# Kernel tuning notes

Hardware: AMD Instinct MI355X
Metric: run time of the kernel (lower is better)

## Reference

```python
import jax, jax.numpy as jnp
import numpy as np
import math

N = 1500; E = 24000; C_IN = 16; H = 64; NUM_LAYERS = 10; RATIO = 0.9
NEG = -1e9


def setup_inputs() -> dict:
    key = jax.random.key(0)
    ks = jax.random.split(key, 40)
    it = iter(range(40))
    def nrm(shape, scale=0.1):
        return jax.random.normal(ks[next(it)], shape, dtype=jnp.float32) * scale
    src = jax.random.randint(ks[next(it)], (E,), 0, N, dtype=jnp.int32)
    off = jax.random.randint(ks[next(it)], (E,), 1, N, dtype=jnp.int32)
    dst = (src + off) % N  # no self loops in the raw edge list
    return dict(
        x=nrm((N, C_IN), 1.0),
        edge_src=src, edge_dst=dst,
        W1=nrm((C_IN, H // 2)), b1=jnp.zeros((H // 2,), jnp.float32),
        W2=nrm((H // 2, H)), b2=jnp.zeros((H,), jnp.float32),
        W3=nrm((H, H)), b3=jnp.zeros((H,), jnp.float32),
        Wrel=nrm((NUM_LAYERS - 1, H, H)), brel=jnp.zeros((NUM_LAYERS - 1, H), jnp.float32),
        Wroot=nrm((NUM_LAYERS - 1, H, H)),
        pW=nrm((4, H, H)), pb=jnp.zeros((4, H), jnp.float32),
        leW1=nrm((4, H, 1)), leb1=jnp.zeros((4, 1), jnp.float32),
        leW2=nrm((4, H, 1)),
        leW3=nrm((4, H, 1)), leb3=jnp.zeros((4, 1), jnp.float32),
        linW1=nrm((NUM_LAYERS * H, H)), linb1=jnp.zeros((H,), jnp.float32),
        linW2=nrm((H, 10)), linb2=jnp.zeros((10,), jnp.float32),
    )


def _seg_mean(vals, idx, n):
    s = jax.ops.segment_sum(vals, idx, num_segments=n)
    c = jax.ops.segment_sum(jnp.ones((idx.shape[0],), vals.dtype), idx, num_segments=n)
    return s / jnp.maximum(c, 1.0)[:, None]


def _feast(x, W, b, srcL, dstL, n):
    # FeaStConv with heads=1: softmax over a single head == 1 -> mean of lin(x_j) + bias
    return _seg_mean((x @ W)[srcL], dstL, n) + b


def _gconv_sparse(x, src, dst, Wr, br, Wo, n):
    return _seg_mean(x[src], dst, n) @ Wr + br + x @ Wo


def _gconv_dense(x, A, Wr, br, Wo):
    # mean aggregation: divide weighted sum by count of (nonzero) in-edges
    Mf = (A != 0).astype(x.dtype)
    agg = (A.T @ x) / jnp.maximum(Mf.sum(0), 1.0)[:, None]
    return agg @ Wr + br + x @ Wo


def _topk_pool(xc, fitness, ratio):
    k = int(math.ceil(ratio * xc.shape[0]))
    fit_k, perm = jax.lax.top_k(fitness, k)
    return xc[perm] * fit_k[:, None], perm


def _asap_sparse(x, src, dst, pW, pb, leW1, leb1, leW2, leW3, leb3):
    n = x.shape[0]
    ar = jnp.arange(n, dtype=src.dtype)
    srcL = jnp.concatenate([src, ar])  # add remaining self loops (weight 1)
    dstL = jnp.concatenate([dst, ar])
    xq = jax.ops.segment_max(x[srcL], dstL, num_segments=n) @ pW + pb
    s = jax.nn.leaky_relu(jnp.sum(xq[dstL] * x[srcL], -1), 0.2)
    m = jax.ops.segment_max(s, dstL, num_segments=n)
    e = jnp.exp(s - m[dstL])
    score = e / jax.ops.segment_sum(e, dstL, num_segments=n)[dstL]
    xc = jax.ops.segment_sum(x[srcL] * score[:, None], dstL, num_segments=n)
    # LEConv fitness score (edge weight = 1)
    a = xc @ leW1 + leb1
    b = xc @ leW2
    agg = jax.ops.segment_sum(a[srcL] - b[dstL], dstL, num_segments=n)
    fitness = jax.nn.sigmoid((agg + xc @ leW3 + leb3)[:, 0])
    x_new, perm = _topk_pool(xc, fitness, RATIO)
    S = jnp.zeros((n, n), x.dtype).at[srcL, dstL].add(score)
    A = jnp.zeros((n, n), x.dtype).at[srcL, dstL].add(1.0)
    Sp = S[:, perm]
    A_new = Sp.T @ A @ Sp
    k = A_new.shape[0]
    return x_new, A_new * (1.0 - jnp.eye(k, dtype=x.dtype))  # remove diag


def _asap_dense(x, A, pW, pb, leW1, leb1, leW2, leW3, leb3):
    n = x.shape[0]
    A = A + jnp.diag((jnp.diag(A) == 0).astype(A.dtype))  # add remaining self loops
    M = A != 0
    Mf = M.astype(x.dtype)
    xq = jnp.max(jnp.where(M[:, :, None], x[:, None, :], NEG), axis=0) @ pW + pb  # [n,H]
    Sc = jnp.where(M, jax.nn.leaky_relu(x @ xq.T, 0.2), NEG)  # [j,i]
    m = Sc.max(0)
    e = jnp.where(M, jnp.exp(Sc - m), 0.0)
    score = e / e.sum(0)
    xc = score.T @ x
    a = xc @ leW1 + leb1
    b = xc @ leW2
    agg = Mf.T @ a - Mf.sum(0)[:, None] * b
    fitness = jax.nn.sigmoid((agg + xc @ leW3 + leb3)[:, 0])
    x_new, perm = _topk_pool(xc, fitness, RATIO)
    Sp = score[:, perm]
    A_new = Sp.T @ A @ Sp
    k = A_new.shape[0]
    return x_new, A_new * (1.0 - jnp.eye(k, dtype=x.dtype))


def _forward(x, edge_src, edge_dst, W1, b1, W2, b2, W3, b3, Wrel, brel, Wroot,
             pW, pb, leW1, leb1, leW2, leW3, leb3, linW1, linb1, linW2, linb2):
    n = x.shape[0]
    ar = jnp.arange(n, dtype=edge_src.dtype)
    srcL = jnp.concatenate([edge_src, ar])  # FeaStConv add_self_loops=True
    dstL = jnp.concatenate([edge_dst, ar])
    x = jax.nn.elu(_feast(x, W1, b1, srcL, dstL, n))
    x = jax.nn.elu(_feast(x, W2, b2, srcL, dstL, n))
    x = jax.nn.elu(_feast(x, W3, b3, srcL, dstL, n))
    xs = [x.mean(0, keepdims=True)]  # single graph -> global_mean_pool == mean
    A = None
    for i in range(NUM_LAYERS - 1):
        if A is None:
            x = jax.nn.relu(_gconv_sparse(x, edge_src, edge_dst, Wrel[i], brel[i], Wroot[i], x.shape[0]))
        else:
            x = jax.nn.relu(_gconv_dense(x, A, Wrel[i], brel[i], Wroot[i]))
        xs.append(x.mean(0, keepdims=True))
        if i % 2 == 0 and i < NUM_LAYERS - 2:
            p = i // 2
            args = (pW[p], pb[p], leW1[p], leb1[p], leW2[p], leW3[p], leb3[p])
            if A is None:
                x, A = _asap_sparse(x, edge_src, edge_dst, *args)
            else:
                x, A = _asap_dense(x, A, *args)
    h = jnp.concatenate(xs, axis=-1)  # [1, NUM_LAYERS*H] jumping-knowledge cat
    h = jax.nn.relu(h @ linW1 + linb1)
    return jax.nn.log_softmax(h @ linW2 + linb2, axis=-1)


def reference(x, edge_src, edge_dst, W1, b1, W2, b2, W3, b3, Wrel, brel, Wroot,
              pW, pb, leW1, leb1, leW2, leW3, leb3, linW1, linb1, linW2, linb2):
    return _forward(x, edge_src, edge_dst, W1, b1, W2, b2, W3, b3, Wrel, brel, Wroot,
                    pW, pb, leW1, leb1, leW2, leW3, leb3, linW1, linb1, linW2, linb2)
```

## Files before the change

### kernel.cpp

```cpp
#include <hip/hip_runtime.h>
#include <math.h>

#define NEGV -1000000000.0f

typedef short short8 __attribute__((ext_vector_type(8)));
typedef float floatx4 __attribute__((ext_vector_type(4)));

__device__ __forceinline__ float sigm(float x){ return 1.0f/(1.0f+expf(-x)); }
__device__ __forceinline__ void edge_sd(int e,const int* src,const int* dst,int E,int& s,int& d){
  if(e<E){ s=src[e]; d=dst[e]; } else { s=e-E; d=s; }
}
__device__ __forceinline__ ushort bf16rn(float x){
  unsigned u = __float_as_uint(x);
  unsigned r = (u + 0x7fffu + ((u>>16)&1u)) >> 16;
  return (ushort)r;
}
__device__ __forceinline__ float bf16f(ushort h){ return __uint_as_float(((unsigned)h)<<16); }

__global__ void k_zero(float* __restrict__ p, size_t n){
  size_t i = (size_t)blockIdx.x*256 + threadIdx.x;
  if (i < n) p[i] = 0.0f;
}

__global__ void k_split3(const float* __restrict__ src,int R,int Cs,int ld,
                         ushort* __restrict__ dst,int Cp,int bmode){
  int idx = blockIdx.x*256+threadIdx.x;
  if (idx >= R*Cp) return;
  int r = idx / Cp, c = idx - r*Cp;
  float x = (c < Cs) ? src[(size_t)r*ld + c] : 0.0f;
  ushort h = bf16rn(x);
  ushort l = bf16rn(x - bf16f(h));
  size_t base = (size_t)r*(3*Cp) + c;
  dst[base]        = h;
  dst[base + Cp]   = bmode ? l : h;
  dst[base + 2*Cp] = bmode ? h : l;
}
__global__ void k_split3_Tdual(const float* __restrict__ src,int Rs,int Cs,int ld,
                               const int* __restrict__ gperm,const float* __restrict__ cscale,
                               const float* __restrict__ emax,
                               ushort* __restrict__ dstA,ushort* __restrict__ dstB,
                               ushort* __restrict__ dstCpad,int Kp){
  __shared__ float t[32][33];
  int tx = threadIdx.x & 31, ty = threadIdx.x >> 5;
  int kb = blockIdx.y*32, xb = blockIdx.x*32;
  int x = xb + tx;
  int gx = (x < Cs) ? gperm[x] : 0;
#pragma unroll
  for (int i=0;i<4;i++){
    int k = kb + ty + i*8;
    t[ty+i*8][tx] = (k < Rs && x < Cs) ? src[(size_t)k*ld + gx] : 0.0f;
  }
  __syncthreads();
  const int K3 = 3*Kp;
#pragma unroll
  for (int i=0;i<4;i++){
    int xo = xb + ty + i*8, ko = kb + tx;
    if (xo < Cs){
      float v = 0.0f;
      if (ko < Rs){
        int g = gperm[xo];
        v = expf(t[tx][ty+i*8] - emax[g]) * cscale[g];
      }
      ushort h = bf16rn(v);
      ushort l = bf16rn(v - bf16f(h));
      size_t base = (size_t)xo*K3 + ko;
      dstA[base] = h; dstA[base+Kp] = h; dstA[base+2*Kp] = l;
      dstB[base] = h; dstB[base+Kp] = l; dstB[base+2*Kp] = h;
      if (ko >= Rs){ dstCpad[base]=0; dstCpad[base+Kp]=0; dstCpad[base+2*Kp]=0; }
    }
  }
}

template<int EPI>
__global__ __launch_bounds__(256) void k_gemm_mfma(
    const ushort* __restrict__ A, const ushort* __restrict__ B,
    float* __restrict__ C, int ldc, int M, int N, int K3,
    const float* __restrict__ mask, int ldm)
{
  __shared__ ushort As[2][64][72];
  __shared__ ushort Bs[2][64][72];
  const int tid = threadIdx.x;
  const int m0 = blockIdx.y*64, n0 = blockIdx.x*64;
  const int w = tid>>6, lane = tid&63;
  const int lo4 = lane&15, quad = lane>>4;
  const int sr = tid>>2, sseg = tid&3;

  floatx4 acc[4];
#pragma unroll
  for(int c=0;c<4;c++){ acc[c][0]=0.f; acc[c][1]=0.f; acc[c][2]=0.f; acc[c][3]=0.f; }

  const size_t arow = (size_t)(m0+sr)*K3;
  const size_t brow = (size_t)(n0+sr)*K3;
  const bool aval = (m0+sr) < M;
  const bool bval = (n0+sr) < N;

  uint4 av0 = make_uint4(0,0,0,0), av1 = make_uint4(0,0,0,0);
  uint4 bv0 = make_uint4(0,0,0,0), bv1 = make_uint4(0,0,0,0);
  if (aval){ av0 = *(const uint4*)(A + arow + sseg*8);
             av1 = *(const uint4*)(A + arow + 32 + sseg*8); }
  if (bval){ bv0 = *(const uint4*)(B + brow + sseg*8);
             bv1 = *(const uint4*)(B + brow + 32 + sseg*8); }
  *(uint4*)&As[0][sr][sseg*8] = av0; *(uint4*)&As[0][sr][32+sseg*8] = av1;
  *(uint4*)&Bs[0][sr][sseg*8] = bv0; *(uint4*)&Bs[0][sr][32+sseg*8] = bv1;
  __syncthreads();

  const int T = K3 >> 6;
  for (int i=0;i<T;i++){
    const int cb = i & 1;
    if (i+1 < T){
      const int k0 = (i+1)<<6;
      av0 = make_uint4(0,0,0,0); av1 = make_uint4(0,0,0,0);
      bv0 = make_uint4(0,0,0,0); bv1 = make_uint4(0,0,0,0);
      if (aval){ av0 = *(const uint4*)(A + arow + k0 + sseg*8);
                 av1 = *(const uint4*)(A + arow + k0 + 32 + sseg*8); }
      if (bval){ bv0 = *(const uint4*)(B + brow + k0 + sseg*8);
                 bv1 = *(const uint4*)(B + brow + k0 + 32 + sseg*8); }
    }
    short8 af0 = *(const short8*)&As[cb][16*w + lo4][quad*8];
    short8 af1 = *(const short8*)&As[cb][16*w + lo4][32+quad*8];
#pragma unroll
    for (int c=0;c<4;c++){
      short8 bf0 = *(const short8*)&Bs[cb][16*c + lo4][quad*8];
      acc[c] = __builtin_amdgcn_mfma_f32_16x16x32_bf16(af0, bf0, acc[c], 0, 0, 0);
      short8 bf1 = *(const short8*)&Bs[cb][16*c + lo4][32+quad*8];
      acc[c] = __builtin_amdgcn_mfma_f32_16x16x32_bf16(af1, bf1, acc[c], 0, 0, 0);
    }
    if (i+1 < T){
      __syncthreads();
      *(uint4*)&As[1-cb][sr][sseg*8] = av0; *(uint4*)&As[1-cb][sr][32+sseg*8] = av1;
      *(uint4*)&Bs[1-cb][sr][sseg*8] = bv0; *(uint4*)&Bs[1-cb][sr][32+sseg*8] = bv1;
      __syncthreads();
    }
  }

#pragma unroll
  for (int c=0;c<4;c++){
    const int gn = n0 + 16*c + lo4;
#pragma unroll
    for (int r=0;r<4;r++){
      const int gm = m0 + 16*w + quad*4 + r;
      if (gm < M && gn < N){
        float v = acc[c][r];
        if (EPI==1) v = (mask[(size_t)gm*ldm+gn] != 0.0f || gm==gn) ? (v > 0.0f ? v : 0.2f*v) : NEGV;
        if (EPI==2 && gm==gn) v = 0.0f;
        C[(size_t)gm*ldc+gn] = v;
      }
    }
  }
}

__global__ __launch_bounds__(256) void k_gemm_mfma_tb(
    const ushort* __restrict__ A, const ushort* __restrict__ B,
    ushort* __restrict__ Cb, int Kp, int M, int N, int K3)
{
  __shared__ ushort As[2][64][72];
  __shared__ ushort Bs[2][64][72];
  const int tid = threadIdx.x;
  const int m0 = blockIdx.y*64, n0 = blockIdx.x*64;
  const int w = tid>>6, lane = tid&63;
  const int lo4 = lane&15, quad = lane>>4;
  const int sr = tid>>2, sseg = tid&3;

  floatx4 acc[4];
#pragma unroll
  for(int c=0;c<4;c++){ acc[c][0]=0.f; acc[c][1]=0.f; acc[c][2]=0.f; acc[c][3]=0.f; }

  const size_t arow = (size_t)(m0+sr)*K3;
  const size_t brow = (size_t)(n0+sr)*K3;
  const bool aval = (m0+sr) < M;
  const bool bval = (n0+sr) < N;

  uint4 av0 = make_uint4(0,0,0,0), av1 = make_uint4(0,0,0,0);
  uint4 bv0 = make_uint4(0,0,0,0), bv1 = make_uint4(0,0,0,0);
  if (aval){ av0 = *(const uint4*)(A + arow + sseg*8);
             av1 = *(const uint4*)(A + arow + 32 + sseg*8); }
  if (bval){ bv0 = *(const uint4*)(B + brow + sseg*8);
             bv1 = *(const uint4*)(B + brow + 32 + sseg*8); }
  *(uint4*)&As[0][sr][sseg*8] = av0; *(uint4*)&As[0][sr][32+sseg*8] = av1;
  *(uint4*)&Bs[0][sr][sseg*8] = bv0; *(uint4*)&Bs[0][sr][32+sseg*8] = bv1;
  __syncthreads();

  const int T = K3 >> 6;
  for (int i=0;i<T;i++){
    const int cb = i & 1;
    if (i+1 < T){
      const int k0 = (i+1)<<6;
      av0 = make_uint4(0,0,0,0); av1 = make_uint4(0,0,0,0);
      bv0 = make_uint4(0,0,0,0); bv1 = make_uint4(0,0,0,0);
      if (aval){ av0 = *(const uint4*)(A + arow + k0 + sseg*8);
                 av1 = *(const uint4*)(A + arow + k0 + 32 + sseg*8); }
      if (bval){ bv0 = *(const uint4*)(B + brow + k0 + sseg*8);
                 bv1 = *(const uint4*)(B + brow + k0 + 32 + sseg*8); }
    }
    short8 af0 = *(const short8*)&As[cb][16*w + lo4][quad*8];
    short8 af1 = *(const short8*)&As[cb][16*w + lo4][32+quad*8];
#pragma unroll
    for (int c=0;c<4;c++){
      short8 bf0 = *(const short8*)&Bs[cb][16*c + lo4][quad*8];
      acc[c] = __builtin_amdgcn_mfma_f32_16x16x32_bf16(af0, bf0, acc[c], 0, 0, 0);
      short8 bf1 = *(const short8*)&Bs[cb][16*c + lo4][32+quad*8];
      acc[c] = __builtin_amdgcn_mfma_f32_16x16x32_bf16(af1, bf1, acc[c], 0, 0, 0);
    }
    if (i+1 < T){
      __syncthreads();
      *(uint4*)&As[1-cb][sr][sseg*8] = av0; *(uint4*)&As[1-cb][sr][32+sseg*8] = av1;
      *(uint4*)&Bs[1-cb][sr][sseg*8] = bv0; *(uint4*)&Bs[1-cb][sr][32+sseg*8] = bv1;
      __syncthreads();
    }
  }

  const int K3o = 3*Kp;
#pragma unroll
  for (int c=0;c<4;c++){
    const int gn = n0 + 16*c + lo4;
    if (gn < N){
#pragma unroll
      for (int r=0;r<4;r++){
        const int gm = m0 + 16*w + quad*4 + r;
        if (gm < M){
          size_t base = (size_t)gn*K3o + gm;
          float sp = bf16f(B[base]) + bf16f(B[base+Kp]);
          float v = acc[c][r] + sp;
          ushort h = bf16rn(v);
          ushort l = bf16rn(v - bf16f(h));
          Cb[base] = h; Cb[base+Kp] = l; Cb[base+2*Kp] = h;
        }
      }
    }
  }
}

template<bool MAXM, bool COUNT, bool EXPM, bool SELF>
__global__ __launch_bounds__(256) void k_skinny(
    const float* __restrict__ A, int lda,
    const float* __restrict__ X,
    const float* __restrict__ mcol,
    float* __restrict__ P, int* __restrict__ cntp,
    int M, int K, int kchunk)
{
  __shared__ float As[16][68];
  __shared__ float Xs[16][68];
  const int tid = threadIdx.x;
  const int m0 = blockIdx.y * 64;
  const int tmb = (tid & 15) * 4, tnb = (tid >> 4) * 4;
  float acc[4][4];
  int cacc[4] = {0,0,0,0};
#pragma unroll
  for (int i=0;i<4;i++)
#pragma unroll
    for (int j=0;j<4;j++) acc[i][j] = MAXM ? NEGV : 0.0f;

  const int kstart = blockIdx.z * kchunk;
  int kend = kstart + kchunk; if (kend > K) kend = K;
  const int ml = tid & 63, tb = tid >> 6;
  const bool mvalid = (m0 + ml) < M;
  float mc = 0.0f;
  if (EXPM && mvalid) mc = mcol[m0 + ml];

  for (int k0 = kstart; k0 < kend; k0 += 16) {
#pragma unroll
    for (int s=0;s<4;s++) {
      const int tk = tb + s*4;
      float va = 0.0f, vx = 0.0f;
      if ((k0+tk) < K) {
        if (mvalid){
          va = A[(size_t)(k0+tk)*lda + m0 + ml];
          if (EXPM) va = expf(va - mc);
        }
        vx = X[(size_t)(k0+tk)*64 + ml];
      }
      As[tk][ml] = va;
      Xs[tk][ml] = vx;
    }
    __syncthreads();
#pragma unroll
    for (int kk=0; kk<16; kk++) {
      const float4 a4 = *(const float4*)&As[kk][tmb];
      const float4 b4 = *(const float4*)&Xs[kk][tnb];
      const float av[4] = {a4.x,a4.y,a4.z,a4.w};
      const float bv[4] = {b4.x,b4.y,b4.z,b4.w};
#pragma unroll
      for (int i=0;i<4;i++){
        if (COUNT) cacc[i] += (av[i] != 0.0f) ? 1 : 0;
#pragma unroll
        for (int j=0;j<4;j++) {
          if (MAXM) acc[i][j] = fmaxf(acc[i][j], av[i] != 0.0f ? bv[j] : NEGV);
          else      acc[i][j] = fmaf(av[i], bv[j], acc[i][j]);
        }
      }
    }
    __syncthreads();
  }

  const size_t slab = (size_t)blockIdx.z * M * 64;
#pragma unroll
  for (int i=0;i<4;i++){
    const int m = m0 + tmb + i;
    if (m < M){
#pragma unroll
      for (int j=0;j<4;j++){
        float v = acc[i][j];
        if (SELF) v = fmaxf(v, X[(size_t)m*64 + tnb + j]);
        P[slab + (size_t)m*64 + tnb + j] = v;
      }
    }
  }
  if (COUNT && tnb == 0){
#pragma unroll
    for (int i=0;i<4;i++){
      const int m = m0 + tmb + i;
      if (m < M) cntp[blockIdx.z*M + m] = cacc[i];
    }
  }
}

__global__ __launch_bounds__(256) void k_poolq(
    const float* __restrict__ SEGP,const int* __restrict__ cntp8,int Z,
    const float* __restrict__ pWp,const float* __restrict__ pbp,
    const float* __restrict__ X,
    ushort* __restrict__ dstA,ushort* __restrict__ dstB,
    float* __restrict__ cntP,int n)
{
  __shared__ float xq[4][65];
  const int tid = threadIdx.x;
  const int r = tid>>6, j = tid&63;
  const int i = blockIdx.x*4 + r;
  float v = NEGV;
  if (i < n){
    for(int z=0;z<Z;z++) v = fmaxf(v, SEGP[(size_t)z*n*64 + (size_t)i*64 + j]);
    if (j == 0){
      int c=1; for(int z=0;z<Z;z++) c += cntp8[z*n+i];
      cntP[i] = (float)c;
    }
  }
  xq[r][j] = v;
  __syncthreads();
  if (i < n){
    float s = pbp[j];
    for(int q=0;q<64;q++) s = fmaf(xq[r][q], pWp[q*64+j], s);
    size_t base = (size_t)i*192 + j;
    ushort h = bf16rn(s), l = bf16rn(s - bf16f(h));
    dstB[base] = h; dstB[base+64] = l; dstB[base+128] = h;
    float x = X[(size_t)i*64 + j];
    h = bf16rn(x); l = bf16rn(x - bf16f(h));
    dstA[base] = h; dstA[base+64] = h; dstA[base+128] = l;
  }
}

__global__ __launch_bounds__(256) void k_gconv_fuse(
    const float* __restrict__ SEGP,const int* __restrict__ cntp8,int Z,
    const float* __restrict__ Wrel,const float* __restrict__ brel,
    const float* __restrict__ X,const float* __restrict__ Wroot,
    float* __restrict__ XN,int n,float* __restrict__ meanacc,float inv_n)
{
  __shared__ float agg_s[4][65];
  __shared__ float xrow[4][65];
  __shared__ float cnt_s[4];
  const int tid = threadIdx.x;
  const int r = tid>>6, j = tid&63;
  const int i = blockIdx.x*4 + r;
  float a = 0.0f;
  if (i < n){
    for(int z=0;z<Z;z++) a += SEGP[(size_t)z*n*64 + (size_t)i*64 + j];
    xrow[r][j] = X[(size_t)i*64 + j];
    if (j == 0){
      int c=0; for(int z=0;z<Z;z++) c += cntp8[z*n+i];
      cnt_s[r] = (float)(c>1?c:1);
    }
  }
  agg_s[r][j] = a;
  __syncthreads();
  float v = 0.0f;
  if (i < n){
    float acc=0.0f, rt=0.0f;
    for(int q=0;q<64;q++){
      acc = fmaf(agg_s[r][q], Wrel[q*64+j], acc);
      rt  = fmaf(xrow[r][q],  Wroot[q*64+j], rt);
    }
    v = fmaxf(acc/cnt_s[r] + brel[j] + rt, 0.0f);
    XN[(size_t)i*64 + j] = v;
  }
  __syncthreads();
  agg_s[r][j] = v;
  __syncthreads();
  if (r == 0) atomicAdd(&meanacc[j], (agg_s[0][j]+agg_s[1][j]+agg_s[2][j]+agg_s[3][j])*inv_n);
}

__global__ __launch_bounds__(256) void k_smax_fused(const float* __restrict__ S,int n,
                                                    float* __restrict__ mcol,float* __restrict__ invd){
  __shared__ float red[16][17];
  const int jc = threadIdx.x & 15, rg = threadIdx.x >> 4;
  const int j = blockIdx.x*16 + jc;
  float m = -3.0e38f;
  if (j < n)
    for(int i=rg;i<n;i+=16) m = fmaxf(m, S[(size_t)i*n+j]);
  red[rg][jc] = m;
  __syncthreads();
  for(int s=8;s>0;s>>=1){
    if(rg<s) red[rg][jc] = fmaxf(red[rg][jc], red[rg+s][jc]);
    __syncthreads();
  }
  const float mc = red[0][jc];
  __syncthreads();
  float sum = 0.0f;
  if (j < n)
    for(int i=rg;i<n;i+=16) sum += expf(S[(size_t)i*n+j]-mc);
  red[rg][jc] = sum;
  __syncthreads();
  for(int s=8;s>0;s>>=1){
    if(rg<s) red[rg][jc] += red[rg+s][jc];
    __syncthreads();
  }
  if(rg==0 && j<n){ mcol[j]=mc; invd[j]=1.0f/red[0][jc]; }
}

__global__ __launch_bounds__(256) void k_xcabc_dense(
    const float* __restrict__ SEGP,int Z,const float* __restrict__ invd,
    float* __restrict__ XC,
    const float* __restrict__ w1,const float* bb1,const float* __restrict__ w2,
    const float* __restrict__ w3,const float* bb3,
    float* aN,float* bN,float* cN,int* pcnt,int n)
{
  __shared__ float xc[4][65];
  const int tid = threadIdx.x;
  const int r = tid>>6, j = tid&63;
  const int i = blockIdx.x*4 + r;
  if (blockIdx.x==0 && tid==0) *pcnt = 0;
  float v = 0.0f;
  if (i < n){
    for(int z=0;z<Z;z++) v += SEGP[(size_t)z*n*64 + (size_t)i*64 + j];
    v *= invd[i];
    XC[(size_t)i*64+j] = v;
  }
  xc[r][j] = v;
  __syncthreads();
  if (i < n && j < 3){
    float s = (j==0)?bb1[0]:((j==2)?bb3[0]:0.0f);
    const float* w = (j==0)?w1:((j==1)?w2:w3);
    for(int q=0;q<64;q++) s = fmaf(xc[r][q], w[q], s);
    if(j==0) aN[i]=s; else if(j==1) bN[i]=s; else cN[i]=s;
  }
}

__global__ void k_aggcol(const float* __restrict__ A,const float* __restrict__ aN,
                         float* __restrict__ aggp,int n){
  int idx = blockIdx.x*256+threadIdx.x; if(idx>=n*16) return;
  int j = idx % n, c = idx / n;
  int i0 = (int)(((long long)n*c)/16), i1 = (int)(((long long)n*(c+1))/16);
  float s = 0.0f;
  for(int i=i0;i<i1;i++) if(A[(size_t)i*n + j] != 0.0f) s += aN[i];
  aggp[c*n + j] = s;
}

template<int MODE>
__global__ __launch_bounds__(256) void k_rank_fused(
    const float* __restrict__ fit_in,
    const float* __restrict__ aggp,const float* __restrict__ cntP,
    const float* __restrict__ aN,const float* __restrict__ bN,const float* __restrict__ cN,
    const float* __restrict__ XC,float* __restrict__ XN,
    int n,int k,int* pcnt,int* perm)
{
  __shared__ float fs[1504];
  const int tid = threadIdx.x;
  for(int u=tid; u<n; u+=256){
    float f;
    if (MODE==0) f = fit_in[u];
    else {
      float a = aN[u];
      for(int c=0;c<16;c++) a += aggp[c*n+u];
      f = sigm(a - cntP[u]*bN[u] + cN[u]);
    }
    fs[u] = f;
  }
  __syncthreads();
  const int v = blockIdx.x*256+tid; if(v>=n) return;
  const float fv = fs[v]; int r = 0;
  for(int u=0;u<n;u++){ float fu = fs[u]; r += (fu > fv || (fu == fv && u < v)) ? 1 : 0; }
  if (r < k){
    int p = atomicAdd(pcnt,1);
    perm[p] = v;
    const float* src = XC + (size_t)v*64;
    float* d = XN + (size_t)p*64;
    for(int h=0;h<64;h++) d[h] = src[h]*fv;
  }
}

__global__ void k_deg(const int* __restrict__ src,const int* __restrict__ dst,int* indeg,int* outdeg,int E){
  int e = blockIdx.x*256+threadIdx.x; if(e>=E) return;
  atomicAdd(&indeg[dst[e]],1); atomicAdd(&outdeg[src[e]],1);
}
__global__ __launch_bounds__(256) void k_prefix2(const int* __restrict__ indeg,const int* __restrict__ outdeg,
                          int* offD,int* curD,int* offS,int* curS,int n){
  __shared__ int ds[1504];
  const int* dsrc = blockIdx.y ? outdeg : indeg;
  for(int u=threadIdx.x; u<n; u+=256) ds[u] = dsrc[u];
  __syncthreads();
  int t = blockIdx.x*256+threadIdx.x; if(t>n) return;
  int s = 0;
  for(int u=0;u<t;u++) s += ds[u]+1;
  if (blockIdx.y){ offS[t]=s; if(t<n) curS[t]=s; }
  else           { offD[t]=s; if(t<n) curD[t]=s; }
}
__global__ void k_csr_fill2(const int* src,const int* dst,
                            int* curS,int* colS,int* eidS,
                            int* curD,int* rowD,int* eidD,int E,int n){
  int e = blockIdx.x*256+threadIdx.x; if(e>=E+n) return;
  int s,d; edge_sd(e,src,dst,E,s,d);
  int p = atomicAdd(&curS[s],1); colS[p]=d; eidS[p]=e;
  int q = atomicAdd(&curD[d],1); rowD[q]=s; eidD[q]=e;
}

__global__ void k_mm_small(const float* __restrict__ A,const float* __restrict__ W,
                           const float* __restrict__ b,float* __restrict__ C,
                           int M,int K,int Np,int act){
  int idx = blockIdx.x*256+threadIdx.x; if(idx>=M*Np) return;
  int m = idx/Np, j = idx - m*Np;
  float s = b ? b[j] : 0.0f;
  const float* a = A + (size_t)m*K;
  for(int q=0;q<K;q++) s = fmaf(a[q], W[(size_t)q*Np + j], s);
  if(act==1) s = fmaxf(s, 0.0f);
  C[idx] = s;
}

__global__ void k_feast_gf(const float* __restrict__ Y,const int* __restrict__ offD,
                           const int* __restrict__ rowD,
                           const float* __restrict__ b,float* X,int n,int H,
                           float* __restrict__ meanacc,float inv_n){
  __shared__ float ms[4][64];
  int idx = blockIdx.x*256+threadIdx.x;
  float v = 0.0f;
  if(idx<n*H){
    int i = idx/H, h = idx - i*H;
    int p0 = offD[i], p1 = offD[i+1];
    float s = 0.0f;
    for(int p=p0;p<p1;p++) s += Y[(size_t)rowD[p]*H + h];
    float t = s/(float)(p1-p0) + b[h];
    v = t > 0.0f ? t : (expf(t)-1.0f);
    X[idx] = v;
  }
  if(meanacc){
    int r = threadIdx.x>>6, j = threadIdx.x&63;
    ms[r][j] = (idx<n*H) ? v : 0.0f;
    __syncthreads();
    if(r==0) atomicAdd(&meanacc[j], (ms[0][j]+ms[1][j]+ms[2][j]+ms[3][j])*inv_n);
  }
}

__global__ __launch_bounds__(256) void k_gconv_sparse_f(
    const float* __restrict__ X,const int* __restrict__ offD,const int* __restrict__ rowD,
    const int* __restrict__ eidD,int E,
    const float* __restrict__ Wrel,const float* __restrict__ brel,
    const float* __restrict__ Wroot,
    float* __restrict__ XN,int n,float* __restrict__ meanacc,float inv_n)
{
  __shared__ float agg_s[4][65];
  __shared__ float xrow[4][65];
  __shared__ float cnt_s[4];
  const int tid = threadIdx.x;
  const int r = tid>>6, j = tid&63;
  const int i = blockIdx.x*4 + r;
  float a = 0.0f;
  if (i < n){
    int p0 = offD[i], p1 = offD[i+1], c = 0;
    for(int p=p0;p<p1;p++){
      if (eidD[p] < E){ a += X[(size_t)rowD[p]*64 + j]; c++; }
    }
    xrow[r][j] = X[(size_t)i*64 + j];
    if (j == 0) cnt_s[r] = (float)(c>1?c:1);
  }
  agg_s[r][j] = a;
  __syncthreads();
  float v = 0.0f;
  if (i < n){
    float acc=0.0f, rt=0.0f;
    for(int q=0;q<64;q++){
      acc = fmaf(agg_s[r][q], Wrel[q*64+j], acc);
      rt  = fmaf(xrow[r][q],  Wroot[q*64+j], rt);
    }
    v = fmaxf(acc/cnt_s[r] + brel[j] + rt, 0.0f);
    XN[(size_t)i*64 + j] = v;
  }
  __syncthreads();
  agg_s[r][j] = v;
  __syncthreads();
  if (r == 0) atomicAdd(&meanacc[j], (agg_s[0][j]+agg_s[1][j]+agg_s[2][j]+agg_s[3][j])*inv_n);
}

__global__ __launch_bounds__(256) void k_xqmaxq(
    const float* __restrict__ X,const int* __restrict__ offD,const int* __restrict__ rowD,
    const float* __restrict__ pWp,const float* __restrict__ pbp,
    float* __restrict__ XQ2,int n)
{
  __shared__ float xq[4][65];
  const int tid = threadIdx.x;
  const int r = tid>>6, j = tid&63;
  const int i = blockIdx.x*4 + r;
  float v = -3.0e38f;
  if (i < n){
    int p0 = offD[i], p1 = offD[i+1];
    for(int p=p0;p<p1;p++) v = fmaxf(v, X[(size_t)rowD[p]*64 + j]);
  }
  xq[r][j] = v;
  __syncthreads();
  if (i < n){
    float s = pbp[j];
    for(int q=0;q<64;q++) s = fmaf(xq[r][q], pWp[q*64+j], s);
    XQ2[(size_t)i*64+j] = s;
  }
}

__global__ void k_edge_score(const int* __restrict__ src,const int* __restrict__ dst,
                             const float* __restrict__ XQ2,const float* __restrict__ X,
                             float* sE,int E,int n){
  int e = blockIdx.x*256+threadIdx.x; if(e>=E+n) return;
  int s,d; edge_sd(e,src,dst,E,s,d);
  const float* q = XQ2 + (size_t)d*64;
  const float* x = X + (size_t)s*64;
  float acc = 0.0f;
  for(int h=0;h<64;h++) acc = fmaf(q[h], x[h], acc);
  sE[e] = acc > 0.0f ? acc : 0.2f*acc;
}

__global__ void k_dstsoft(const int* __restrict__ offD,const int* __restrict__ eidD,
                          const float* __restrict__ sE,float* __restrict__ scE,int n){
  int i = blockIdx.x*256+threadIdx.x; if(i>=n) return;
  int p0 = offD[i], p1 = offD[i+1];
  float m = -3.0e38f;
  for(int p=p0;p<p1;p++) m = fmaxf(m, sE[eidD[p]]);
  float d = 0.0f;
  for(int p=p0;p<p1;p++) d += expf(sE[eidD[p]]-m);
  float inv = 1.0f/d;
  for(int p=p0;p<p1;p++){ int e = eidD[p]; scE[e] = expf(sE[e]-m)*inv; }
}

__global__ __launch_bounds__(256) void k_xcabc0(
    const int* __restrict__ offD,const int* __restrict__ rowD,const int* __restrict__ eidD,
    const float* __restrict__ scE,const float* __restrict__ X,
    float* __restrict__ XC,
    const float* __restrict__ w1,const float* bb1,const float* __restrict__ w2,
    const float* __restrict__ w3,const float* bb3,
    float* aN,float* bN,float* cN,int* pcnt,int n)
{
  __shared__ float xc[4][65];
  const int tid = threadIdx.x;
  const int r = tid>>6, j = tid&63;
  const int i = blockIdx.x*4 + r;
  if (blockIdx.x==0 && tid==0) *pcnt = 0;
  float v = 0.0f;
  if (i < n){
    int p0 = offD[i], p1 = offD[i+1];
    for(int p=p0;p<p1;p++) v += scE[eidD[p]] * X[(size_t)rowD[p]*64 + j];
    XC[(size_t)i*64+j] = v;
  }
  xc[r][j] = v;
  __syncthreads();
  if (i < n && j < 3){
    float s = (j==0)?bb1[0]:((j==2)?bb3[0]:0.0f);
    const float* w = (j==0)?w1:((j==1)?w2:w3);
    for(int q=0;q<64;q++) s = fmaf(xc[r][q], w[q], s);
    if(j==0) aN[i]=s; else if(j==1) bN[i]=s; else cN[i]=s;
  }
}

__global__ void k_aggfit0(const int* __restrict__ offD,const int* __restrict__ rowD,
                          const float* aN,const float* bN,const float* cN,
                          float* fit,int n){
  int i = blockIdx.x*256+threadIdx.x; if(i>=n) return;
  int p0 = offD[i], p1 = offD[i+1];
  float s = 0.0f;
  for(int p=p0;p<p1;p++) s += aN[rowD[p]];
  fit[i] = sigm(s - (float)(p1-p0)*bN[i] + cN[i]);
}

__global__ void k_stage1n(const int* src,const int* dst,const int* __restrict__ offS,
                          const int* __restrict__ colS,const int* __restrict__ eidS,
                          const float* __restrict__ scE,
                          float* R,int E,int n){
  int e = blockIdx.x*256+threadIdx.x; if(e>=E+n) return;
  int i,j; edge_sd(e,src,dst,E,i,j);
  int p0 = offS[j], p1 = offS[j+1];
  float* Ri = R + (size_t)i*n;
  for(int p=p0;p<p1;p++) atomicAdd(&Ri[colS[p]], scE[eidS[p]]);
}
__global__ void k_stage2p(const int* __restrict__ perm,const int* __restrict__ offD,
                          const int* __restrict__ rowD,const int* __restrict__ eidD,
                          const float* __restrict__ scE,
                          const float* __restrict__ R,float* A,int k,int n){
  int idx = blockIdx.x*256+threadIdx.x; if(idx>=k*k) return;
  int u = idx/k, v = idx - u*k;
  int d = perm[u], pv = perm[v];
  float acc = 0.0f;
  int p0 = offD[d], p1 = offD[d+1];
  for(int p=p0;p<p1;p++) acc = fmaf(scE[eidD[p]], R[(size_t)rowD[p]*n + pv], acc);
  A[idx] = (u==v) ? 0.0f : acc;
}

__global__ void k_head2(const float* __restrict__ xs,const float* __restrict__ W1,
                        const float* __restrict__ b1,const float* __restrict__ W2,
                        const float* __restrict__ b2,float* out){
  __shared__ float h2[64];
  __shared__ float lg[10];
  int t = threadIdx.x;
  float s = b1[t];
  for(int q=0;q<640;q++) s = fmaf(xs[q], W1[q*64+t], s);
  h2[t] = fmaxf(s, 0.0f);
  __syncthreads();
  if(t < 10){
    float s2 = b2[t];
    for(int k=0;k<64;k++) s2 = fmaf(h2[k], W2[k*10+t], s2);
    lg[t] = s2;
  }
  __syncthreads();
  if(t == 0){
    float mx = lg[0];
    for(int i=1;i<10;i++) mx = fmaxf(mx, lg[i]);
    float se = 0.0f;
    for(int i=0;i<10;i++) se += expf(lg[i]-mx);
    float lse = mx + logf(se);
    for(int i=0;i<10;i++) out[i] = lg[i]-lse;
  }
}

extern "C" void kernel_launch(void* const* d_in, const int* in_sizes, int n_in,
                              void* d_out, int out_size, void* d_ws, size_t ws_size,
                              hipStream_t stream) {
  const int N0 = 1500, E = 24000, Z = 16, L = E + N0;
  const float* x0   = (const float*)d_in[0];
  const int* esrc   = (const int*)d_in[1];
  const int* edst   = (const int*)d_in[2];
  const float* W1   = (const float*)d_in[3];  const float* b1   = (const float*)d_in[4];
  const float* W2   = (const float*)d_in[5];  const float* b2   = (const float*)d_in[6];
  const float* W3   = (const float*)d_in[7];  const float* b3   = (const float*)d_in[8];
  const float* Wrel = (const float*)d_in[9];  const float* brel = (const float*)d_in[10];
  const float* Wroot= (const float*)d_in[11];
  const float* pW   = (const float*)d_in[12]; const float* pb   = (const float*)d_in[13];
  const float* leW1 = (const float*)d_in[14]; const float* leb1 = (const float*)d_in[15];
  const float* leW2 = (const float*)d_in[16]; const float* leW3 = (const float*)d_in[17];
  const float* leb3 = (const float*)d_in[18];
  const float* linW1= (const float*)d_in[19]; const float* linb1= (const float*)d_in[20];
  const float* linW2= (const float*)d_in[21]; const float* linb2= (const float*)d_in[22];
  float* out = (float*)d_out;

  float* ws = (float*)d_ws;
  size_t cur = 0;
  auto allocF = [&](size_t nf)->float*{ float* p = ws + cur; cur += (nf + 15) & ~(size_t)15; return p; };
  float* xs   = allocF(640);
  int* indeg  = (int*)allocF(1504);
  int* outdeg = (int*)allocF(1504);
  float* Xa  = allocF(96000); float* Xb  = allocF(96000); float* Y   = allocF(96000);
  float* XQ2 = allocF(96000); float* XC  = allocF(96000);
  float* mcol = allocF(1504); float* invd = allocF(1504);
  float* aN = allocF(1504); float* bN = allocF(1504); float* cN = allocF(1504);
  float* fit = allocF(1504); float* cntP = allocF(1504);
  int* pcnt = (int*)allocF(16);
  int* perm = (int*)allocF(1504);
  int* offD = (int*)allocF(1504); int* offS = (int*)allocF(1504);
  int* curD = (int*)allocF(1504); int* curS = (int*)allocF(1504);
  int* colS = (int*)allocF(25504); int* eidS = (int*)allocF(25504);
  int* rowD = (int*)allocF(25504); int* eidD = (int*)allocF(25504);
  float* sE = allocF(25504); float* scE = allocF(25504);
  int* cntp8 = (int*)allocF(16*1504);
  float* aggp = allocF(16*1504);
  float* SEGP = allocF((size_t)Z*1504*64);
  float* Rbig = allocF((size_t)1500*1500);
  float* SCb  = Rbig;
  float* A0  = allocF((size_t)1350*1350);
  float* A1s = allocF((size_t)1350*1350);
  const size_t BFSZ = (size_t)1350*4224/2 + 32;
  ushort* Abf = (ushort*)allocF(BFSZ);
  ushort* Bbf = (ushort*)allocF(BFSZ);
  ushort* Cbf = (ushort*)allocF(BFSZ);
  ushort* Dbf = (ushort*)allocF(BFSZ);

  dim3 B256(256);
  auto G1 = [&](size_t n){ return dim3((unsigned)((n + 255) / 256)); };
  auto ZF = [&](void* p, size_t nfloats){ k_zero<<<G1(nfloats),B256,0,stream>>>((float*)p, nfloats); };
  auto kcz = [&](int K){ return (int)(((K + Z*16 - 1) / (Z*16)) * 16); };

  ZF(xs, 640 + 1504 + 1504);
  k_deg<<<G1(E),B256,0,stream>>>(esrc, edst, indeg, outdeg, E);
  k_prefix2<<<dim3((N0+256)/256,2),B256,0,stream>>>(indeg, outdeg, offD, curD, offS, curS, N0);
  k_csr_fill2<<<G1(L),B256,0,stream>>>(esrc, edst, curS, colS, eidS, curD, rowD, eidD, E, N0);

  auto feast = [&](const float* xin,int cin,const float* W,const float* bb,int hh,float* xout,float* macc){
    k_mm_small<<<G1((size_t)N0*hh),B256,0,stream>>>(xin, W, nullptr, Y, N0, cin, hh, 0);
    k_feast_gf<<<G1((size_t)N0*hh),B256,0,stream>>>(Y, offD, rowD, bb, xout, N0, hh, macc, 1.0f/N0);
  };
  feast(x0, 16, W1, b1, 32, Xa, nullptr);
  feast(Xa, 32, W2, b2, 64, Xb, nullptr);
  feast(Xb, 64, W3, b3, 64, Xa, xs + 0);
  float* X = Xa; float* XN = Xb;

  k_gconv_sparse_f<<<dim3((N0+3)/4),B256,0,stream>>>(X, offD, rowD, eidD, E, Wrel, brel, Wroot,
                                                     XN, N0, xs + 64, 1.0f/N0);
  { float* t = X; X = XN; XN = t; }

  {
    const int n = 1500, kk = 1350;
    k_xqmaxq<<<dim3((n+3)/4),B256,0,stream>>>(X, offD, rowD, pW, pb, XQ2, n);
    k_edge_score<<<G1(L),B256,0,stream>>>(esrc, edst, XQ2, X, sE, E, n);
    k_dstsoft<<<G1(n),B256,0,stream>>>(offD, eidD, sE, scE, n);
    k_xcabc0<<<dim3((n+3)/4),B256,0,stream>>>(offD, rowD, eidD, scE, X, XC,
                                              leW1, leb1, leW2, leW3, leb3, aN, bN, cN, pcnt, n);
    k_aggfit0<<<G1(n),B256,0,stream>>>(offD, rowD, aN, bN, cN, fit, n);
    k_rank_fused<0><<<G1(n),B256,0,stream>>>(fit, nullptr, nullptr, nullptr, nullptr, nullptr,
                                             XC, XN, n, kk, pcnt, perm);
    ZF(Rbig, (size_t)n*n);
    k_stage1n<<<G1(L),B256,0,stream>>>(esrc, edst, offS, colS, eidS, scE, Rbig, E, n);
    k_stage2p<<<G1((size_t)kk*kk),B256,0,stream>>>(perm, offD, rowD, eidD, scE, Rbig, A0, kk, n);
    { float* t = X; X = XN; XN = t; }
  }

  float* Acur = A0; float* Aoth = A1s;
  int nn = 1350;

  auto gconv_dense = [&](int layer){
    dim3 g(1, (nn+63)/64, Z);
    k_skinny<false,true,false,false><<<g,B256,0,stream>>>(Acur, nn, X, nullptr, SEGP, cntp8, nn, nn, kcz(nn));
    k_gconv_fuse<<<dim3((nn+3)/4),B256,0,stream>>>(SEGP, cntp8, Z,
        Wrel + (size_t)layer*4096, brel + layer*64, X, Wroot + (size_t)layer*4096,
        XN, nn, xs + (size_t)(layer+1)*64, 1.0f/nn);
    { float* t = X; X = XN; XN = t; }
  };

  auto asap_dense = [&](int kk, int p){
    {
      dim3 g(1, (nn+63)/64, Z);
      k_skinny<true,true,false,true><<<g,B256,0,stream>>>(Acur, nn, X, nullptr, SEGP, cntp8, nn, nn, kcz(nn));
    }
    k_poolq<<<dim3((nn+3)/4),B256,0,stream>>>(SEGP, cntp8, Z, pW + (size_t)p*4096, pb + p*64,
                                              X, Abf, Bbf, cntP, nn);
    {
      dim3 g((nn+63)/64, (nn+63)/64);
      k_gemm_mfma<1><<<g,B256,0,stream>>>(Abf, Bbf, SCb, nn, nn, nn, 192, Acur, nn);
    }
    k_smax_fused<<<dim3((nn+15)/16),B256,0,stream>>>(SCb, nn, mcol, invd);
    {
      dim3 g(1, (nn+63)/64, Z);
      k_skinny<false,false,true,false><<<g,B256,0,stream>>>(SCb, nn, X, mcol, SEGP, nullptr, nn, nn, kcz(nn));
    }
    k_xcabc_dense<<<dim3((nn+3)/4),B256,0,stream>>>(SEGP, Z, invd, XC,
        leW1 + p*64, leb1 + p, leW2 + p*64, leW3 + p*64, leb3 + p, aN, bN, cN, pcnt, nn);
    k_aggcol<<<G1((size_t)nn*16),B256,0,stream>>>(Acur, aN, aggp, nn);
    k_rank_fused<1><<<G1(nn),B256,0,stream>>>(nullptr, aggp, cntP, aN, bN, cN,
                                              XC, XN, nn, kk, pcnt, perm);
    const int Kp = (nn + 63) & ~63;
    const int K3 = 3*Kp;
    k_split3<<<G1((size_t)nn*Kp),B256,0,stream>>>(Acur, nn, nn, nn, Abf, Kp, 0);
    { dim3 gt((kk+31)/32, Kp/32);
      k_split3_Tdual<<<gt,B256,0,stream>>>(SCb, nn, kk, nn, perm, invd, mcol, Dbf, Bbf, Cbf, Kp); }
    { dim3 g((kk+63)/64, (nn+63)/64);
      k_gemm_mfma_tb<<<g,B256,0,stream>>>(Abf, Bbf, Cbf, Kp, nn, kk, K3); }
    { dim3 g((kk+63)/64, (kk+63)/64);
      k_gemm_mfma<2><<<g,B256,0,stream>>>(Dbf, Cbf, Aoth, kk, kk, kk, K3, nullptr, 0); }
    { float* t = X; X = XN; XN = t; }
    { float* t = Acur; Acur = Aoth; Aoth = t; }
    nn = kk;
  };

  gconv_dense(1);
  gconv_dense(2);
  asap_dense(1215, 1);
  gconv_dense(3);
  gconv_dense(4);
  asap_dense(1094, 2);
  gconv_dense(5);
  gconv_dense(6);
  asap_dense(985, 3);
  gconv_dense(7);
  gconv_dense(8);

  k_head2<<<1,64,0,stream>>>(xs, linW1, linb1, linW2, linb2, out);
}
```

Before: 1.514 ms.

## Split-K the dense pooling GEMMs into three partials with separate reduce epilogues

The two bf16 MFMA GEMMs that build the coarsened adjacency now split their K dimension (the three bf16 split components) across gridDim.z = 3. Each slice writes fp32 partials to a new workspace buffer, and small epilogue kernels sum them: one re-splits into hi/lo bf16 for the next GEMM, the other transposes and zeros the diagonal to form the new adjacency. The goal is more blocks in flight for GEMMs that give only about 400 tiles, at the cost of extra partial-buffer traffic and two more launches. The Z split count for the skinny segment kernels also goes from 16 to 32.

New measurement: 1.549 ms. 2.3% more time.

```diff
diff --git a/kernel.cpp b/kernel.cpp
--- a/kernel.cpp
+++ b/kernel.cpp
@@ -142,16 +142,15 @@
       if (gm < M && gn < N){
         float v = acc[c][r];
         if (EPI==1) v = (mask[(size_t)gm*ldm+gn] != 0.0f || gm==gn) ? (v > 0.0f ? v : 0.2f*v) : NEGV;
-        if (EPI==2 && gm==gn) v = 0.0f;
         C[(size_t)gm*ldc+gn] = v;
       }
     }
   }
 }
 
-__global__ __launch_bounds__(256) void k_gemm_mfma_tb(
+__global__ __launch_bounds__(256) void k_gemm_mfma_z(
     const ushort* __restrict__ A, const ushort* __restrict__ B,
-    ushort* __restrict__ Cb, int Kp, int M, int N, int K3)
+    float* __restrict__ P, size_t MN, int M, int N, int K3, int itersZ)
 {
   __shared__ ushort As[2][64][72];
   __shared__ ushort Bs[2][64][72];
@@ -170,20 +169,26 @@
   const bool aval = (m0+sr) < M;
   const bool bval = (n0+sr) < N;
 
+  const int Ttot = K3 >> 6;
+  const int i0 = blockIdx.z * itersZ;
+  int i1 = i0 + itersZ; if (i1 > Ttot) i1 = Ttot;
+
   uint4 av0 = make_uint4(0,0,0,0), av1 = make_uint4(0,0,0,0);
   uint4 bv0 = make_uint4(0,0,0,0), bv1 = make_uint4(0,0,0,0);
-  if (aval){ av0 = *(const uint4*)(A + arow + sseg*8);
-             av1 = *(const uint4*)(A + arow + 32 + sseg*8); }
-  if (bval){ bv0 = *(const uint4*)(B + brow + sseg*8);
-             bv1 = *(const uint4*)(B + brow + 32 + sseg*8); }
+  {
+    const int k0 = i0<<6;
+    if (aval){ av0 = *(const uint4*)(A + arow + k0 + sseg*8);
+               av1 = *(const uint4*)(A + arow + k0 + 32 + sseg*8); }
+    if (bval){ bv0 = *(const uint4*)(B + brow + k0 + sseg*8);
+               bv1 = *(const uint4*)(B + brow + k0 + 32 + sseg*8); }
+  }
   *(uint4*)&As[0][sr][sseg*8] = av0; *(uint4*)&As[0][sr][32+sseg*8] = av1;
   *(uint4*)&Bs[0][sr][sseg*8] = bv0; *(uint4*)&Bs[0][sr][32+sseg*8] = bv1;
   __syncthreads();
 
-  const int T = K3 >> 6;
-  for (int i=0;i<T;i++){
-    const int cb = i & 1;
-    if (i+1 < T){
+  for (int i=i0;i<i1;i++){
+    const int cb = (i-i0) & 1;
+    if (i+1 < i1){
       const int k0 = (i+1)<<6;
       av0 = make_uint4(0,0,0,0); av1 = make_uint4(0,0,0,0);
       bv0 = make_uint4(0,0,0,0); bv1 = make_uint4(0,0,0,0);
@@ -201,7 +206,7 @@
       short8 bf1 = *(const short8*)&Bs[cb][16*c + lo4][32+quad*8];
       acc[c] = __builtin_amdgcn_mfma_f32_16x16x32_bf16(af1, bf1, acc[c], 0, 0, 0);
     }
-    if (i+1 < T){
+    if (i+1 < i1){
       __syncthreads();
       *(uint4*)&As[1-cb][sr][sseg*8] = av0; *(uint4*)&As[1-cb][sr][32+sseg*8] = av1;
       *(uint4*)&Bs[1-cb][sr][sseg*8] = bv0; *(uint4*)&Bs[1-cb][sr][32+sseg*8] = bv1;
@@ -209,7 +214,7 @@
     }
   }
 
-  const int K3o = 3*Kp;
+  float* Pz = P + (size_t)blockIdx.z * MN;
 #pragma unroll
   for (int c=0;c<4;c++){
     const int gn = n0 + 16*c + lo4;
@@ -217,16 +222,44 @@
 #pragma unroll
       for (int r=0;r<4;r++){
         const int gm = m0 + 16*w + quad*4 + r;
-        if (gm < M){
-          size_t base = (size_t)gn*K3o + gm;
-          float sp = bf16f(B[base]) + bf16f(B[base+Kp]);
-          float v = acc[c][r] + sp;
-          ushort h = bf16rn(v);
-          ushort l = bf16rn(v - bf16f(h));
-          Cb[base] = h; Cb[base+Kp] = l; Cb[base+2*Kp] = h;
-        }
+        if (gm < M) Pz[(size_t)gn*M + gm] = acc[c][r];
       }
     }
+  }
+}
+
+__global__ void k_tb_epi(const float* __restrict__ P, size_t MN,
+                         const ushort* __restrict__ Bbf, ushort* __restrict__ Cb,
+                         int Kp, int M){
+  int gm = blockIdx.x*256+threadIdx.x;
+  int gn = blockIdx.y;
+  if (gm >= M) return;
+  const int K3o = 3*Kp;
+  size_t pidx = (size_t)gn*M + gm;
+  float v = P[pidx] + P[MN+pidx] + P[2*MN+pidx];
+  size_t base = (size_t)gn*K3o + gm;
+  v += bf16f(Bbf[base]) + bf16f(Bbf[base+Kp]);
+  ushort h = bf16rn(v), l = bf16rn(v - bf16f(h));
+  Cb[base] = h; Cb[base+Kp] = l; Cb[base+2*Kp] = h;
+}
+
+__global__ __launch_bounds__(256) void k_anew_epi(const float* __restrict__ P, size_t MN,
+                                                  float* __restrict__ Aout, int kk){
+  __shared__ float t[32][33];
+  int tx = threadIdx.x & 31, ty = threadIdx.x >> 5;
+  int ub = blockIdx.x*32, vb = blockIdx.y*32;
+#pragma unroll
+  for(int i=0;i<4;i++){
+    int v = vb+ty+i*8, u = ub+tx;
+    float s = 0.0f;
+    if (v<kk && u<kk){ size_t p = (size_t)v*kk+u; s = P[p]+P[MN+p]+P[2*MN+p]; }
+    t[ty+i*8][tx] = s;
+  }
+  __syncthreads();
+#pragma unroll
+  for(int i=0;i<4;i++){
+    int u = ub+ty+i*8, v = vb+tx;
+    if (u<kk && v<kk) Aout[(size_t)u*kk+v] = (u==v) ? 0.0f : t[tx][ty+i*8];
   }
 }
 
@@ -724,7 +757,7 @@
 extern "C" void kernel_launch(void* const* d_in, const int* in_sizes, int n_in,
                               void* d_out, int out_size, void* d_ws, size_t ws_size,
                               hipStream_t stream) {
-  const int N0 = 1500, E = 24000, Z = 16, L = E + N0;
+  const int N0 = 1500, E = 24000, Z = 32, L = E + N0;
   const float* x0   = (const float*)d_in[0];
   const int* esrc   = (const int*)d_in[1];
   const int* edst   = (const int*)d_in[2];
@@ -759,9 +792,10 @@
   int* colS = (int*)allocF(25504); int* eidS = (int*)allocF(25504);
   int* rowD = (int*)allocF(25504); int* eidD = (int*)allocF(25504);
   float* sE = allocF(25504); float* scE = allocF(25504);
-  int* cntp8 = (int*)allocF(16*1504);
+  int* cntp8 = (int*)allocF((size_t)Z*1504);
   float* aggp = allocF(16*1504);
   float* SEGP = allocF((size_t)Z*1504*64);
+  float* PZ   = allocF((size_t)3*1350*1350);
   float* Rbig = allocF((size_t)1500*1500);
   float* SCb  = Rbig;
   float* A0  = allocF((size_t)1350*1350);
@@ -846,13 +880,18 @@
                                               XC, XN, nn, kk, pcnt, perm);
     const int Kp = (nn + 63) & ~63;
     const int K3 = 3*Kp;
+    const int itersZ = Kp >> 6;
     k_split3<<<G1((size_t)nn*Kp),B256,0,stream>>>(Acur, nn, nn, nn, Abf, Kp, 0);
     { dim3 gt((kk+31)/32, Kp/32);
       k_split3_Tdual<<<gt,B256,0,stream>>>(SCb, nn, kk, nn, perm, invd, mcol, Dbf, Bbf, Cbf, Kp); }
-    { dim3 g((kk+63)/64, (nn+63)/64);
-      k_gemm_mfma_tb<<<g,B256,0,stream>>>(Abf, Bbf, Cbf, Kp, nn, kk, K3); }
-    { dim3 g((kk+63)/64, (kk+63)/64);
-      k_gemm_mfma<2><<<g,B256,0,stream>>>(Dbf, Cbf, Aoth, kk, kk, kk, K3, nullptr, 0); }
+    { dim3 g((kk+63)/64, (nn+63)/64, 3);
+      k_gemm_mfma_z<<<g,B256,0,stream>>>(Abf, Bbf, PZ, (size_t)kk*nn, nn, kk, K3, itersZ); }
+    { dim3 ge((nn+255)/256, kk);
+      k_tb_epi<<<ge,B256,0,stream>>>(PZ, (size_t)kk*nn, Bbf, Cbf, Kp, nn); }
+    { dim3 g((kk+63)/64, (kk+63)/64, 3);
+      k_gemm_mfma_z<<<g,B256,0,stream>>>(Dbf, Cbf, PZ, (size_t)kk*kk, kk, kk, K3, itersZ); }
+    { dim3 ge((kk+31)/32, (kk+31)/32);
+      k_anew_epi<<<ge,B256,0,stream>>>(PZ, (size_t)kk*kk, Aoth, kk); }
     { float* t = X; X = XN; XN = t; }
     { float* t = Acur; Acur = Aoth; Aoth = t; }
     nn = kk;
```
